# Optimization experiments

Measured on AMD Instinct MI355X. Metric: run time of the kernel, lower is better.

The kernel has to match this reference:

```python
import jax, jax.numpy as jnp
import numpy as np

B, N, E = 2, 30000, 120000
IN_F, OUT_F, H = 512, 512, 4
D = OUT_F // H  # head_dim = 128
LN_EPS = 1e-5


def setup_inputs() -> dict:
    key = jax.random.key(0)
    k1, k2, k3, k4 = jax.random.split(key, 4)
    node_features = jax.random.normal(k1, (B, N, IN_F), dtype=jnp.float32)
    edge_index = jax.random.randint(k2, (2, E), 0, N, dtype=jnp.int64)
    # per-head linear transforms (bias=False): W[h] is [in_features, head_dim]
    W = jax.random.normal(k3, (H, IN_F, D), dtype=jnp.float32) / np.sqrt(IN_F)
    # per-head attention vectors a[h] is [2*head_dim] (Linear(2*head_dim,1,bias=False))
    a = jax.random.normal(k4, (H, 2 * D), dtype=jnp.float32) / np.sqrt(2 * D)
    ln_gamma = jnp.ones((OUT_F,), dtype=jnp.float32)
    ln_beta = jnp.zeros((OUT_F,), dtype=jnp.float32)
    return {"node_features": node_features, "edge_index": edge_index,
            "W": W, "a": a, "ln_gamma": ln_gamma, "ln_beta": ln_beta}


def reference(node_features, edge_index, W, a, ln_gamma, ln_beta):
    src, dst = edge_index[0], edge_index[1]
    # all-heads linear transform: [B, H, N, D]
    t = jnp.einsum('bni,hid->bhnd', node_features, W)
    # per-edge gathered features: [B, H, E, D]
    sf = t[:, :, src, :]
    df = t[:, :, dst, :]
    # attention score = [sf ; df] . a  == sf.a_src + df.a_dst  -> [B, H, E]
    scores = (jnp.einsum('bhed,hd->bhe', sf, a[:, :D])
              + jnp.einsum('bhed,hd->bhe', df, a[:, D:]))
    scores = jax.nn.leaky_relu(scores, negative_slope=0.2)
    # NOTE: faithful to source — softmax over ALL edges (dim=-1), not per-dst
    w = jax.nn.softmax(scores, axis=-1)
    # scatter-add aggregation into destination nodes (the Python-loop in torch)
    agg = jnp.zeros_like(t).at[:, :, dst, :].add(w[..., None] * sf)  # [B,H,N,D]
    # concat heads along feature dim (head order preserved)
    out = jnp.transpose(agg, (0, 2, 1, 3)).reshape(node_features.shape[0], N, H * D)
    # LayerNorm over last dim
    mu = jnp.mean(out, axis=-1, keepdims=True)
    var = jnp.mean(jnp.square(out - mu), axis=-1, keepdims=True)
    out = (out - mu) * jax.lax.rsqrt(var + LN_EPS) * ln_gamma + ln_beta
    return out
```

## Files before the change

kernel.cpp:

```cpp
#include <hip/hip_runtime.h>
#include <stdint.h>

#define Bn 2
#define Nn 30000
#define En 120000
#define KIN 512
#define Hh 4
#define Dd 128
#define MROWS 60000
#define MPAD  60032
#define LNEPS 1e-5f
#define EBLK 469

typedef unsigned short u16;
typedef unsigned int   u32;
typedef __attribute__((ext_vector_type(8))) short short8;
typedef __attribute__((ext_vector_type(4))) float f32x4;

__device__ __forceinline__ u16 f2bf(float f) {
    u32 u = __builtin_bit_cast(u32, f);
    u32 r = u + 0x7FFFu + ((u >> 16) & 1u);
    return (u16)(r >> 16);
}
__device__ __forceinline__ float bflo(u32 u) {
    return __builtin_bit_cast(float, u << 16);
}
__device__ __forceinline__ float bfhi(u32 u) {
    return __builtin_bit_cast(float, u & 0xFFFF0000u);
}
__device__ __forceinline__ void ld16(void* lds, const void* g) {
    __builtin_amdgcn_global_load_lds((const __attribute__((address_space(1))) void*)g,
                                     (__attribute__((address_space(3))) void*)lds, 16, 0, 0);
}

#define CVTX_BLKS 15008
#define CVTW_BLKS 1024
__global__ void prep_kernel(const float* __restrict__ x, u16* __restrict__ xb,
                            const float* __restrict__ W, u16* __restrict__ wbt,
                            const int* __restrict__ ei, int* __restrict__ deg) {
    int blk = blockIdx.x;
    if (blk < CVTX_BLKS) {
        long base = ((long)blk * 256 + threadIdx.x) * 8;
        short8 o = {};
        if (base < (long)MROWS * KIN) {
            const float4* px = (const float4*)(x + base);
            float4 v0 = px[0], v1 = px[1];
            o[0] = (short)f2bf(v0.x); o[1] = (short)f2bf(v0.y);
            o[2] = (short)f2bf(v0.z); o[3] = (short)f2bf(v0.w);
            o[4] = (short)f2bf(v1.x); o[5] = (short)f2bf(v1.y);
            o[6] = (short)f2bf(v1.z); o[7] = (short)f2bf(v1.w);
        }
        *(short8*)(xb + base) = o;
    } else if (blk < CVTX_BLKS + CVTW_BLKS) {
        int idx = (blk - CVTX_BLKS) * 256 + threadIdx.x;
        int c = idx >> 9, i = idx & 511;
        int h = c >> 7, d = c & 127;
        wbt[idx] = f2bf(W[h * (KIN * Dd) + i * Dd + d]);
    } else {
        int e = (blk - CVTX_BLKS - CVTW_BLKS) * 256 + threadIdx.x;
        if (e < En) atomicAdd(&deg[ei[En + e]], 1);
    }
}

__device__ void scan256(const int* __restrict__ deg, int* __restrict__ offs,
                        int* __restrict__ cursor) {
    __shared__ int part[256];
    int tid = threadIdx.x;
    const int CH = 118;
    int start = tid * CH;
    int s = 0;
    for (int i = 0; i < CH; i++) {
        int n = start + i;
        if (n < Nn) s += deg[n];
    }
    part[tid] = s;
    __syncthreads();
    for (int off = 1; off < 256; off <<= 1) {
        int xv = (tid >= off) ? part[tid - off] : 0;
        __syncthreads();
        part[tid] += xv;
        __syncthreads();
    }
    int run = part[tid] - s;
    for (int i = 0; i < CH; i++) {
        int n = start + i;
        if (n < Nn) {
            offs[n] = run;
            cursor[n] = run;
            run += deg[n];
        }
    }
    if (tid == 255) offs[Nn] = part[255];
}

__launch_bounds__(256)
__global__ void gemm(const u16* __restrict__ xb, const u16* __restrict__ wbt,
                     const float* __restrict__ ag, u16* __restrict__ t,
                     float* __restrict__ s1g, float* __restrict__ s2g,
                     const int* __restrict__ deg, int* __restrict__ offs,
                     int* __restrict__ cursor) {
    if (blockIdx.y == 469) {
        if (blockIdx.x == 0) scan256(deg, offs, cursor);
        return;
    }
    __shared__ __align__(16) u16 As[128 * 32];
    __shared__ __align__(16) u16 Bs[128 * 32];
    __shared__ float sred[2][2][128];
    const int tid = threadIdx.x;
    const int m0 = blockIdx.y * 128, n0 = blockIdx.x * 128;
    const int w = tid >> 6, l = tid & 63;
    const int wr = (w >> 1) * 64, wc = (w & 1) * 64;
    const int lr = l & 15, lk = l >> 4;
    f32x4 acc[4][4] = {};

    for (int k0 = 0; k0 < KIN; k0 += 32) {
        #pragma unroll
        for (int inst = 0; inst < 2; inst++) {
            int q = inst * 256 + tid;
            const u16* gap = xb  + (long)(m0 + (q >> 2)) * KIN + k0 + (q & 3) * 8;
            const u16* gbp = wbt + (long)(n0 + (q >> 2)) * KIN + k0 + (q & 3) * 8;
            ld16(&As[q * 8], gap);
            ld16(&Bs[q * 8], gbp);
        }
        __syncthreads();
        short8 af[4], bfr[4];
        #pragma unroll
        for (int mi = 0; mi < 4; mi++)
            af[mi] = *(const short8*)&As[(wr + mi * 16 + lr) * 32 + lk * 8];
        #pragma unroll
        for (int nj = 0; nj < 4; nj++)
            bfr[nj] = *(const short8*)&Bs[(wc + nj * 16 + lr) * 32 + lk * 8];
        #pragma unroll
        for (int mi = 0; mi < 4; mi++)
            #pragma unroll
            for (int nj = 0; nj < 4; nj++)
                acc[mi][nj] = __builtin_amdgcn_mfma_f32_16x16x32_bf16(
                    af[mi], bfr[nj], acc[mi][nj], 0, 0, 0);
        __syncthreads();
    }
    #pragma unroll
    for (int mi = 0; mi < 4; mi++)
        #pragma unroll
        for (int r = 0; r < 4; r++) {
            int row = m0 + wr + mi * 16 + lk * 4 + r;
            u16* tp = t + (long)row * 512 + n0 + wc + lr;
            #pragma unroll
            for (int nj = 0; nj < 4; nj++)
                tp[nj * 16] = f2bf(acc[mi][nj][r]);
        }
    const int h = n0 >> 7;
    float a1c[4], a2c[4];
    #pragma unroll
    for (int nj = 0; nj < 4; nj++) {
        int col = wc + nj * 16 + lr;
        a1c[nj] = ag[h * 256 + col];
        a2c[nj] = ag[h * 256 + 128 + col];
    }
    float p1[16], p2[16];
    #pragma unroll
    for (int mi = 0; mi < 4; mi++)
        #pragma unroll
        for (int r = 0; r < 4; r++) {
            float v1 = 0.f, v2 = 0.f;
            #pragma unroll
            for (int nj = 0; nj < 4; nj++) {
                float tv = acc[mi][nj][r];
                v1 += tv * a1c[nj];
                v2 += tv * a2c[nj];
            }
            p1[mi * 4 + r] = v1;
            p2[mi * 4 + r] = v2;
        }
    #pragma unroll
    for (int off = 1; off < 16; off <<= 1)
        #pragma unroll
        for (int i = 0; i < 16; i++) {
            p1[i] += __shfl_xor(p1[i], off, 64);
            p2[i] += __shfl_xor(p2[i], off, 64);
        }
    if (lr == 0)
        #pragma unroll
        for (int mi = 0; mi < 4; mi++)
            #pragma unroll
            for (int r = 0; r < 4; r++) {
                int row = wr + mi * 16 + lk * 4 + r;
                sred[0][w & 1][row] = p1[mi * 4 + r];
                sred[1][w & 1][row] = p2[mi * 4 + r];
            }
    __syncthreads();
    if (tid < 128) {
        int row = m0 + tid;
        if (row < MROWS) {
            s1g[(long)row * 4 + h] = sred[0][0][tid] + sred[0][1][tid];
            s2g[(long)row * 4 + h] = sred[1][0][tid] + sred[1][1][tid];
        }
    }
}

__global__ void edgescatter_kernel(const int* __restrict__ ei, const float* __restrict__ s1,
                                   const float* __restrict__ s2, int* __restrict__ cursor,
                                   int* __restrict__ srcs, float* __restrict__ pw,
                                   float* __restrict__ Zpart) {
    int e = blockIdx.x * 256 + threadIdx.x;
    int tid = threadIdx.x;
    float v[8] = {0.f, 0.f, 0.f, 0.f, 0.f, 0.f, 0.f, 0.f};
    if (e < En) {
        int src = ei[e], dst = ei[En + e];
        #pragma unroll
        for (int b = 0; b < Bn; b++) {
            float4 v1 = *(const float4*)(s1 + ((long)b * Nn + src) * 4);
            float4 v2 = *(const float4*)(s2 + ((long)b * Nn + dst) * 4);
            float s;
            s = v1.x + v2.x; s = s > 0.f ? s : 0.2f * s; v[b * 4 + 0] = __expf(s);
            s = v1.y + v2.y; s = s > 0.f ? s : 0.2f * s; v[b * 4 + 1] = __expf(s);
            s = v1.z + v2.z; s = s > 0.f ? s : 0.2f * s; v[b * 4 + 2] = __expf(s);
            s = v1.w + v2.w; s = s > 0.f ? s : 0.2f * s; v[b * 4 + 3] = __expf(s);
        }
        int pos = atomicAdd(&cursor[dst], 1);
        srcs[pos] = src;
        *(float4*)(pw + (long)pos * 4)        = make_float4(v[0], v[1], v[2], v[3]);
        *(float4*)(pw + ((long)En + pos) * 4) = make_float4(v[4], v[5], v[6], v[7]);
    }
    #pragma unroll
    for (int off = 1; off < 64; off <<= 1)
        #pragma unroll
        for (int i = 0; i < 8; i++)
            v[i] += __shfl_xor(v[i], off, 64);
    __shared__ float red[4][8];
    if ((tid & 63) == 0)
        #pragma unroll
        for (int i = 0; i < 8; i++)
            red[tid >> 6][i] = v[i];
    __syncthreads();
    if (tid < 8)
        Zpart[(long)blockIdx.x * 8 + tid] =
            red[0][tid] + red[1][tid] + red[2][tid] + red[3][tid];
}

__global__ void zreduce_kernel(const float* __restrict__ Zpart, float* __restrict__ invZ) {
    int tid = threadIdx.x;
    int g = tid >> 5, l = tid & 31;
    float s = 0.f;
    for (int i = l; i < EBLK; i += 32)
        s += Zpart[(long)i * 8 + g];
    #pragma unroll
    for (int off = 1; off < 32; off <<= 1)
        s += __shfl_xor(s, off, 64);
    if (l == 0) invZ[g] = 1.0f / s;
}

__launch_bounds__(128)
__global__ void agg_kernel(const u16* __restrict__ t, const int* __restrict__ srcs,
                           const float* __restrict__ pw, const float* __restrict__ invZ,
                           const int* __restrict__ offs,
                           const float* __restrict__ gamma, const float* __restrict__ beta,
                           float* __restrict__ out) {
    int tid = threadIdx.x;
    int n = blockIdx.x;
    int b = blockIdx.y;
    int h = tid >> 5;
    int j0 = offs[n], j1 = offs[n + 1];
    const float* pwb = pw + (long)b * En * 4;
    const u16* tb = t + (long)b * Nn * 512;
    float a0 = 0.f, a1 = 0.f, a2 = 0.f, a3 = 0.f;
    int j = j0;
    for (; j + 4 <= j1; j += 4) {
        int s0 = srcs[j], s1i = srcs[j + 1], s2i = srcs[j + 2], s3i = srcs[j + 3];
        float w0 = pwb[(long)j * 4 + h];
        float w1 = pwb[(long)(j + 1) * 4 + h];
        float w2 = pwb[(long)(j + 2) * 4 + h];
        float w3 = pwb[(long)(j + 3) * 4 + h];
        uint2 r0 = *(const uint2*)(tb + (long)s0 * 512 + tid * 4);
        uint2 r1 = *(const uint2*)(tb + (long)s1i * 512 + tid * 4);
        uint2 r2 = *(const uint2*)(tb + (long)s2i * 512 + tid * 4);
        uint2 r3 = *(const uint2*)(tb + (long)s3i * 512 + tid * 4);
        a0 += w0 * bflo(r0.x) + w1 * bflo(r1.x) + w2 * bflo(r2.x) + w3 * bflo(r3.x);
        a1 += w0 * bfhi(r0.x) + w1 * bfhi(r1.x) + w2 * bfhi(r2.x) + w3 * bfhi(r3.x);
        a2 += w0 * bflo(r0.y) + w1 * bflo(r1.y) + w2 * bflo(r2.y) + w3 * bflo(r3.y);
        a3 += w0 * bfhi(r0.y) + w1 * bfhi(r1.y) + w2 * bfhi(r2.y) + w3 * bfhi(r3.y);
    }
    for (; j < j1; j++) {
        int s0 = srcs[j];
        float w0 = pwb[(long)j * 4 + h];
        uint2 r0 = *(const uint2*)(tb + (long)s0 * 512 + tid * 4);
        a0 += w0 * bflo(r0.x);
        a1 += w0 * bfhi(r0.x);
        a2 += w0 * bflo(r0.y);
        a3 += w0 * bfhi(r0.y);
    }
    float invz = invZ[b * 4 + h];
    a0 *= invz; a1 *= invz; a2 *= invz; a3 *= invz;
    float s  = a0 + a1 + a2 + a3;
    float ss = a0 * a0 + a1 * a1 + a2 * a2 + a3 * a3;
    #pragma unroll
    for (int off = 1; off < 64; off <<= 1) {
        s  += __shfl_xor(s, off, 64);
        ss += __shfl_xor(ss, off, 64);
    }
    __shared__ float red[2][2];
    int wv = tid >> 6;
    if ((tid & 63) == 0) { red[wv][0] = s; red[wv][1] = ss; }
    __syncthreads();
    s  = red[0][0] + red[1][0];
    ss = red[0][1] + red[1][1];
    float mean = s * (1.0f / 512.0f);
    float var = ss * (1.0f / 512.0f) - mean * mean;
    var = var < 0.f ? 0.f : var;
    float scale = rsqrtf(var + LNEPS);
    int c = tid * 4;
    float4 o;
    o.x = (a0 - mean) * scale * gamma[c + 0] + beta[c + 0];
    o.y = (a1 - mean) * scale * gamma[c + 1] + beta[c + 1];
    o.z = (a2 - mean) * scale * gamma[c + 2] + beta[c + 2];
    o.w = (a3 - mean) * scale * gamma[c + 3] + beta[c + 3];
    *(float4*)(out + ((long)b * Nn + n) * 512 + c) = o;
}

extern "C" void kernel_launch(void* const* d_in, const int* in_sizes, int n_in,
                              void* d_out, int out_size, void* d_ws, size_t ws_size,
                              hipStream_t stream) {
    const float* x     = (const float*)d_in[0];
    const int*   ei    = (const int*)d_in[1];
    const float* W     = (const float*)d_in[2];
    const float* a     = (const float*)d_in[3];
    const float* gamma = (const float*)d_in[4];
    const float* beta  = (const float*)d_in[5];
    float* out = (float*)d_out;

    char* ws = (char*)d_ws;
    size_t off = 0;
    auto alloc = [&](size_t bytes) -> void* {
        void* ptr = ws + off;
        off = (off + bytes + 255) & ~(size_t)255;
        return ptr;
    };
    u16*   xb     = (u16*)alloc((size_t)MPAD * KIN * 2);
    u16*   wbt    = (u16*)alloc((size_t)512 * 512 * 2);
    u16*   t      = (u16*)alloc((size_t)MPAD * 512 * 2);
    float* s1     = (float*)alloc((size_t)MROWS * 4 * 4);
    float* s2     = (float*)alloc((size_t)MROWS * 4 * 4);
    float* pw     = (float*)alloc((size_t)Bn * En * 4 * 4);
    float* Zpart  = (float*)alloc((size_t)EBLK * 8 * 4);
    float* invZ   = (float*)alloc(8 * 4);
    int*   deg    = (int*)alloc((size_t)Nn * 4);
    int*   offs   = (int*)alloc((size_t)(Nn + 1) * 4);
    int*   cursor = (int*)alloc((size_t)Nn * 4);
    int*   srcs   = (int*)alloc((size_t)En * 4);

    hipMemsetAsync(deg, 0, (size_t)Nn * 4, stream);

    prep_kernel<<<CVTX_BLKS + CVTW_BLKS + EBLK, 256, 0, stream>>>(x, xb, W, wbt, ei, deg);
    gemm<<<dim3(4, 470), 256, 0, stream>>>(xb, wbt, a, t, s1, s2, deg, offs, cursor);
    edgescatter_kernel<<<EBLK, 256, 0, stream>>>(ei, s1, s2, cursor, srcs, pw, Zpart);
    zreduce_kernel<<<1, 256, 0, stream>>>(Zpart, invZ);
    agg_kernel<<<dim3(Nn, Bn), 128, 0, stream>>>(t, srcs, pw, invZ, offs, gamma, beta, out);
}
```

Measured before the change: 410.5 us.

## Restructure GEMM to full-width 128x512 tiles with double-buffered swizzled LDS

The projection GEMM now gives each 512-thread block a 128-row by 512-column tile covering all four heads, so the A tile is loaded once rather than four times. LDS staging is double-buffered so the next k-slice loads while MFMAs run, and an XOR swizzle is added to reduce bank conflicts. Each wave owns one full head, so the attention-score dot products are written straight to global memory without the shared-memory cross-wave reduction. The prefix scan moves to block 0 with 512 threads. In exchange the block uses more LDS and more accumulator registers (32 MFMA tiles per wave), which may lower occupancy.

```diff
diff --git a/kernel.cpp b/kernel.cpp
--- a/kernel.cpp
+++ b/kernel.cpp
@@ -62,11 +62,11 @@
     }
 }
 
-__device__ void scan256(const int* __restrict__ deg, int* __restrict__ offs,
+__device__ void scan512(const int* __restrict__ deg, int* __restrict__ offs,
                         int* __restrict__ cursor) {
-    __shared__ int part[256];
+    __shared__ int part[512];
     int tid = threadIdx.x;
-    const int CH = 118;
+    const int CH = 59;
     int start = tid * CH;
     int s = 0;
     for (int i = 0; i < CH; i++) {
@@ -75,7 +75,7 @@
     }
     part[tid] = s;
     __syncthreads();
-    for (int off = 1; off < 256; off <<= 1) {
+    for (int off = 1; off < 512; off <<= 1) {
         int xv = (tid >= off) ? part[tid - off] : 0;
         __syncthreads();
         part[tid] += xv;
@@ -90,69 +90,79 @@
             run += deg[n];
         }
     }
-    if (tid == 255) offs[Nn] = part[255];
-}
-
-__launch_bounds__(256)
+    if (tid == 511) offs[Nn] = part[511];
+}
+
+__launch_bounds__(512)
 __global__ void gemm(const u16* __restrict__ xb, const u16* __restrict__ wbt,
                      const float* __restrict__ ag, u16* __restrict__ t,
                      float* __restrict__ s1g, float* __restrict__ s2g,
                      const int* __restrict__ deg, int* __restrict__ offs,
                      int* __restrict__ cursor) {
-    if (blockIdx.y == 469) {
-        if (blockIdx.x == 0) scan256(deg, offs, cursor);
-        return;
-    }
-    __shared__ __align__(16) u16 As[128 * 32];
-    __shared__ __align__(16) u16 Bs[128 * 32];
-    __shared__ float sred[2][2][128];
+    if (blockIdx.x == 0) { scan512(deg, offs, cursor); return; }
+    __shared__ __align__(16) u16 As[2][128 * 32];
+    __shared__ __align__(16) u16 Bs[2][512 * 32];
     const int tid = threadIdx.x;
-    const int m0 = blockIdx.y * 128, n0 = blockIdx.x * 128;
+    const int m0 = (blockIdx.x - 1) * 128;
     const int w = tid >> 6, l = tid & 63;
-    const int wr = (w >> 1) * 64, wc = (w & 1) * 64;
     const int lr = l & 15, lk = l >> 4;
-    f32x4 acc[4][4] = {};
-
-    for (int k0 = 0; k0 < KIN; k0 += 32) {
-        #pragma unroll
-        for (int inst = 0; inst < 2; inst++) {
-            int q = inst * 256 + tid;
-            const u16* gap = xb  + (long)(m0 + (q >> 2)) * KIN + k0 + (q & 3) * 8;
-            const u16* gbp = wbt + (long)(n0 + (q >> 2)) * KIN + k0 + (q & 3) * 8;
-            ld16(&As[q * 8], gap);
-            ld16(&Bs[q * 8], gbp);
+    const int wrM = (w >> 2) * 64;
+    const int h = w & 3;
+    const int wc = h * 128;
+    const int swz = (lk * 8) ^ ((lr & 6) << 2);
+    int aoff[4], boff[8];
+    #pragma unroll
+    for (int mi = 0; mi < 4; mi++) aoff[mi] = (wrM + mi * 16 + lr) * 32 + swz;
+    #pragma unroll
+    for (int nj = 0; nj < 8; nj++) boff[nj] = (wc + nj * 16 + lr) * 32 + swz;
+
+    const int grow = tid >> 2, gslot = tid & 3;
+    const int gsw = (gslot * 8) ^ ((grow & 6) << 2);
+    const u16* agsrc = xb + (long)(m0 + grow) * KIN + gsw;
+    const u16* bgsrc = wbt + (long)grow * KIN + gsw;
+    f32x4 acc[4][8] = {};
+
+    auto STAGE = [&](u16* Ab, u16* Bb, int k0) {
+        ld16(Ab + (long)tid * 8, agsrc + k0);
+        #pragma unroll
+        for (int i = 0; i < 4; i++)
+            ld16(Bb + ((long)(i * 512 + tid)) * 8, bgsrc + (long)i * 128 * KIN + k0);
+    };
+
+    STAGE(As[0], Bs[0], 0);
+    __syncthreads();
+    #pragma unroll 2
+    for (int t16 = 0; t16 < 16; t16++) {
+        u16* Ac = As[t16 & 1];
+        u16* Bc = Bs[t16 & 1];
+        if (t16 < 15) STAGE(As[(t16 + 1) & 1], Bs[(t16 + 1) & 1], (t16 + 1) * 32);
+        short8 af[4];
+        #pragma unroll
+        for (int mi = 0; mi < 4; mi++) af[mi] = *(const short8*)&Ac[aoff[mi]];
+        #pragma unroll
+        for (int nj = 0; nj < 8; nj++) {
+            short8 bv = *(const short8*)&Bc[boff[nj]];
+            #pragma unroll
+            for (int mi = 0; mi < 4; mi++)
+                acc[mi][nj] = __builtin_amdgcn_mfma_f32_16x16x32_bf16(
+                    af[mi], bv, acc[mi][nj], 0, 0, 0);
         }
         __syncthreads();
-        short8 af[4], bfr[4];
-        #pragma unroll
-        for (int mi = 0; mi < 4; mi++)
-            af[mi] = *(const short8*)&As[(wr + mi * 16 + lr) * 32 + lk * 8];
-        #pragma unroll
-        for (int nj = 0; nj < 4; nj++)
-            bfr[nj] = *(const short8*)&Bs[(wc + nj * 16 + lr) * 32 + lk * 8];
-        #pragma unroll
-        for (int mi = 0; mi < 4; mi++)
+    }
+    #pragma unroll
+    for (int mi = 0; mi < 4; mi++)
+        #pragma unroll
+        for (int r = 0; r < 4; r++) {
+            int row = m0 + wrM + mi * 16 + lk * 4 + r;
+            u16* tp = t + (long)row * 512 + wc + lr;
             #pragma unroll
-            for (int nj = 0; nj < 4; nj++)
-                acc[mi][nj] = __builtin_amdgcn_mfma_f32_16x16x32_bf16(
-                    af[mi], bfr[nj], acc[mi][nj], 0, 0, 0);
-        __syncthreads();
-    }
-    #pragma unroll
-    for (int mi = 0; mi < 4; mi++)
-        #pragma unroll
-        for (int r = 0; r < 4; r++) {
-            int row = m0 + wr + mi * 16 + lk * 4 + r;
-            u16* tp = t + (long)row * 512 + n0 + wc + lr;
-            #pragma unroll
-            for (int nj = 0; nj < 4; nj++)
+            for (int nj = 0; nj < 8; nj++)
                 tp[nj * 16] = f2bf(acc[mi][nj][r]);
         }
-    const int h = n0 >> 7;
-    float a1c[4], a2c[4];
-    #pragma unroll
-    for (int nj = 0; nj < 4; nj++) {
-        int col = wc + nj * 16 + lr;
+    float a1c[8], a2c[8];
+    #pragma unroll
+    for (int nj = 0; nj < 8; nj++) {
+        int col = nj * 16 + lr;
         a1c[nj] = ag[h * 256 + col];
         a2c[nj] = ag[h * 256 + 128 + col];
     }
@@ -163,7 +173,7 @@
         for (int r = 0; r < 4; r++) {
             float v1 = 0.f, v2 = 0.f;
             #pragma unroll
-            for (int nj = 0; nj < 4; nj++) {
+            for (int nj = 0; nj < 8; nj++) {
                 float tv = acc[mi][nj][r];
                 v1 += tv * a1c[nj];
                 v2 += tv * a2c[nj];
@@ -178,22 +188,17 @@
             p1[i] += __shfl_xor(p1[i], off, 64);
             p2[i] += __shfl_xor(p2[i], off, 64);
         }
-    if (lr == 0)
+    if (lr == 0) {
         #pragma unroll
         for (int mi = 0; mi < 4; mi++)
             #pragma unroll
             for (int r = 0; r < 4; r++) {
-                int row = wr + mi * 16 + lk * 4 + r;
-                sred[0][w & 1][row] = p1[mi * 4 + r];
-                sred[1][w & 1][row] = p2[mi * 4 + r];
+                int row = m0 + wrM + mi * 16 + lk * 4 + r;
+                if (row < MROWS) {
+                    s1g[(long)row * 4 + h] = p1[mi * 4 + r];
+                    s2g[(long)row * 4 + h] = p2[mi * 4 + r];
+                }
             }
-    __syncthreads();
-    if (tid < 128) {
-        int row = m0 + tid;
-        if (row < MROWS) {
-            s1g[(long)row * 4 + h] = sred[0][0][tid] + sred[0][1][tid];
-            s2g[(long)row * 4 + h] = sred[1][0][tid] + sred[1][1][tid];
-        }
     }
 }
 
@@ -350,7 +355,7 @@
     hipMemsetAsync(deg, 0, (size_t)Nn * 4, stream);
 
     prep_kernel<<<CVTX_BLKS + CVTW_BLKS + EBLK, 256, 0, stream>>>(x, xb, W, wbt, ei, deg);
-    gemm<<<dim3(4, 470), 256, 0, stream>>>(xb, wbt, a, t, s1, s2, deg, offs, cursor);
+    gemm<<<470, 512, 0, stream>>>(xb, wbt, a, t, s1, s2, deg, offs, cursor);
     edgescatter_kernel<<<EBLK, 256, 0, stream>>>(ei, s1, s2, cursor, srcs, pw, Zpart);
     zreduce_kernel<<<1, 256, 0, stream>>>(Zpart, invZ);
     agg_kernel<<<dim3(Nn, Bn), 128, 0, stream>>>(t, srcs, pw, invZ, offs, gamma, beta, out);
```

Result: faster. 396.7 us (-3.4%).
